# Kernel optimization log

Measured on AMD Instinct MI355X. Metric: run time of the kernel, lower is better.

The kernel has to match this reference:

```python
import jax, jax.numpy as jnp
import numpy as np

N, F_IN, HID, EMB, K = 4096, 1433, 256, 16, 10
ALPHA = 0.2   # LeakyReLU negative slope
V = 1.0       # Student-t degrees of freedom
NEG_INF = -9e15


def _xavier(key, shape):
    std = (2.0 / (shape[0] + shape[1])) ** 0.5
    return std * jax.random.normal(key, shape, dtype=jnp.float32)


def setup_inputs() -> dict:
    key = jax.random.key(0)
    ks = jax.random.split(key, 10)
    x = jax.random.normal(ks[0], (N, F_IN), dtype=jnp.float32)
    adj = (jax.random.uniform(ks[1], (N, N)) < 0.01).astype(jnp.float32)
    adj = jnp.maximum(adj, jnp.eye(N, dtype=jnp.float32))
    M = jax.random.uniform(ks[2], (N, N), dtype=jnp.float32)  # proximity matrix
    return {
        "x": x,
        "adj": adj,
        "M": M,
        "W1": _xavier(ks[3], (F_IN, HID)),
        "a_self1": _xavier(ks[4], (HID, 1)),
        "a_neigh1": _xavier(ks[5], (HID, 1)),
        "W2": _xavier(ks[6], (HID, EMB)),
        "a_self2": _xavier(ks[7], (EMB, 1)),
        "a_neigh2": _xavier(ks[8], (EMB, 1)),
        "cluster_layer": _xavier(ks[9], (K, EMB)),
    }


def _gat_layer(h_in, adj, M, W, a_self, a_neigh):
    h = h_in @ W                                   # [N, D]
    # dense attention logits: self score broadcast over rows + neighbor score over cols
    logits = (h @ a_self) + (h @ a_neigh).T        # [N, N]
    logits = jax.nn.leaky_relu(logits * M, negative_slope=ALPHA)
    logits = jnp.where(adj > 0, logits, NEG_INF)
    attention = jax.nn.softmax(logits, axis=1)     # row-stochastic
    return jax.nn.elu(attention @ h)               # concat=True -> ELU


def reference(x, adj, M, W1, a_self1, a_neigh1, W2, a_self2, a_neigh2, cluster_layer):
    h = _gat_layer(x, adj, M, W1, a_self1, a_neigh1)
    h = _gat_layer(h, adj, M, W2, a_self2, a_neigh2)
    # F.normalize(h, p=2, dim=1) with eps clamp
    z = h / jnp.maximum(jnp.linalg.norm(h, axis=1, keepdims=True), 1e-12)
    A_pred = jax.nn.sigmoid(z @ z.T)               # [N, N] dot-product decoder
    # Student-t soft assignment (get_Q)
    dist2 = jnp.sum((z[:, None, :] - cluster_layer[None, :, :]) ** 2, axis=2)  # [N, K]
    q = 1.0 / (1.0 + dist2 / V)
    q = q ** ((V + 1.0) / 2.0)
    q = q / jnp.sum(q, axis=1, keepdims=True)
    return A_pred, z, q
```

## Files before the change

### kernel.cpp

```cpp
#include <hip/hip_runtime.h>
#include <hip/hip_bf16.h>

#define NN 4096
#define FIN 1433
#define HID 256
#define EMB 16
#define KCL 10
#define CAP 256
#define ALPHA_LR 0.2f
#define KP 1472
#define NT (KP / 64)

typedef __attribute__((ext_vector_type(8))) short bf16x8;
typedef __attribute__((ext_vector_type(8))) short s16x8;
typedef __attribute__((ext_vector_type(4))) float f32x4;

__device__ __align__(16) short g_xb[(size_t)NN * KP];
__device__ __align__(16) short g_w1t[(size_t)HID * KP];
__device__ __align__(16) float g_h1[(size_t)NN * HID];
__device__ __align__(16) float g_s1[NN];
__device__ __align__(16) float g_n1[NN];
__device__ __align__(16) int   g_cnt[NN];
__device__ __align__(16) int   g_cols[(size_t)NN * CAP];
__device__ __align__(16) float g_mv[(size_t)NN * CAP];
__device__ __align__(16) float g_h2[(size_t)NN * EMB];
__device__ __align__(16) float g_s2[NN];
__device__ __align__(16) float g_n2[NN];
__device__ __align__(16) float g_z[(size_t)NN * EMB];

__device__ __forceinline__ short f2bf(float f) {
    union { float f; unsigned u; } v; v.f = f;
    unsigned r = v.u + 0x7fffu + ((v.u >> 16) & 1u);
    return (short)(r >> 16);
}
__device__ __forceinline__ float eluf(float v) { return v > 0.f ? v : __expf(v) - 1.f; }

__launch_bounds__(256)
__global__ void k_cast(const float* __restrict__ x, const float* __restrict__ W1) {
    int b = blockIdx.x, tid = threadIdx.x;
    if (b < NN) {
        const float* src = x + (size_t)b * FIN;
        short* dst = g_xb + (size_t)b * KP;
        for (int j = tid; j < KP; j += 256)
            dst[j] = (j < FIN) ? f2bf(src[j]) : (short)0;
    } else {
        int n = b - NN;
        short* dst = g_w1t + (size_t)n * KP;
        for (int k = tid; k < KP; k += 256)
            dst[k] = (k < FIN) ? f2bf(W1[(size_t)k * HID + n]) : (short)0;
    }
}

__launch_bounds__(256)
__global__ void k_gemm1b() {
    __shared__ short As[2][32][72];
    __shared__ short Bs[2][64][72];
    int bid = blockIdx.x;
    int rt = bid >> 2, nt = bid & 3;
    int row0 = rt * 32, n0 = nt * 64;
    int tid = threadIdx.x, lane = tid & 63, w = tid >> 6;
    int wm = w >> 1, wn = w & 1;
    int arow = tid >> 3, acol = (tid & 7) * 8;
    int brow = tid >> 2, bcol = (tid & 3) * 16;
    const short* xptr = g_xb  + (size_t)(row0 + arow) * KP + acol;
    const short* wptr = g_w1t + (size_t)(n0 + brow) * KP + bcol;
    f32x4 acc0 = {0.f,0.f,0.f,0.f}, acc1 = {0.f,0.f,0.f,0.f};

    s16x8 a_r  = *(const s16x8*)xptr;
    s16x8 b_r0 = *(const s16x8*)wptr;
    s16x8 b_r1 = *(const s16x8*)(wptr + 8);
    *(s16x8*)&As[0][arow][acol]     = a_r;
    *(s16x8*)&Bs[0][brow][bcol]     = b_r0;
    *(s16x8*)&Bs[0][brow][bcol + 8] = b_r1;
    __syncthreads();

    int fr = lane & 15, fk = (lane >> 4) * 8;
    for (int t = 0; t < NT; ++t) {
        int cur = t & 1;
        if (t + 1 < NT) {
            a_r  = *(const s16x8*)(xptr + (t + 1) * 64);
            b_r0 = *(const s16x8*)(wptr + (t + 1) * 64);
            b_r1 = *(const s16x8*)(wptr + (t + 1) * 64 + 8);
        }
        #pragma unroll
        for (int kk = 0; kk < 2; ++kk) {
            bf16x8 af  = *(const bf16x8*)&As[cur][wm * 16 + fr][fk + kk * 32];
            bf16x8 bf0 = *(const bf16x8*)&Bs[cur][wn * 32 + fr][fk + kk * 32];
            bf16x8 bf1 = *(const bf16x8*)&Bs[cur][wn * 32 + 16 + fr][fk + kk * 32];
            acc0 = __builtin_amdgcn_mfma_f32_16x16x32_bf16(af, bf0, acc0, 0, 0, 0);
            acc1 = __builtin_amdgcn_mfma_f32_16x16x32_bf16(af, bf1, acc1, 0, 0, 0);
        }
        if (t + 1 < NT) {
            *(s16x8*)&As[cur ^ 1][arow][acol]     = a_r;
            *(s16x8*)&Bs[cur ^ 1][brow][bcol]     = b_r0;
            *(s16x8*)&Bs[cur ^ 1][brow][bcol + 8] = b_r1;
            __syncthreads();
        }
    }
    int rowb = (lane >> 4) * 4;
    #pragma unroll
    for (int t = 0; t < 4; ++t) {
        int grow = row0 + wm * 16 + rowb + t;
        g_h1[(size_t)grow * HID + n0 + wn * 32 + fr]      = acc0[t];
        g_h1[(size_t)grow * HID + n0 + wn * 32 + 16 + fr] = acc1[t];
    }
}

__launch_bounds__(256)
__global__ void k_sn1(const float* __restrict__ a_s, const float* __restrict__ a_n) {
    int row = blockIdx.x * 4 + (threadIdx.x >> 6);
    int lane = threadIdx.x & 63;
    const float* r = g_h1 + (size_t)row * HID;
    float ss = 0.f, sn = 0.f;
    #pragma unroll
    for (int q = 0; q < 4; ++q) {
        float hv = r[lane + 64 * q];
        ss += hv * a_s[lane + 64 * q];
        sn += hv * a_n[lane + 64 * q];
    }
    #pragma unroll
    for (int o = 32; o; o >>= 1) { ss += __shfl_xor(ss, o); sn += __shfl_xor(sn, o); }
    if (lane == 0) { g_s1[row] = ss; g_n1[row] = sn; }
}

__launch_bounds__(256)
__global__ void k_csr(const float* __restrict__ adj, const float* __restrict__ M) {
    __shared__ int lc[4][CAP];
    int w = threadIdx.x >> 6;
    int row = blockIdx.x * 4 + w;
    int lane = threadIdx.x & 63;
    const float* Arow = adj + (size_t)row * NN;
    unsigned long long lmask = (1ull << lane) - 1ull;
    int base = 0;
    #pragma unroll
    for (int it = 0; it < 16; it += 4) {
        int j0 = it * 256 + lane * 4;
        f32x4 A0 = *(const f32x4*)&Arow[j0];
        f32x4 A1 = *(const f32x4*)&Arow[j0 + 256];
        f32x4 A2 = *(const f32x4*)&Arow[j0 + 512];
        f32x4 A3 = *(const f32x4*)&Arow[j0 + 768];
        f32x4 blk[4] = {A0, A1, A2, A3};
        #pragma unroll
        for (int b = 0; b < 4; ++b) {
            #pragma unroll
            for (int q = 0; q < 4; ++q) {
                bool nz = blk[b][q] > 0.f;
                unsigned long long bal = __ballot(nz);
                if (nz) {
                    int pos = base + __popcll(bal & lmask);
                    if (pos < CAP) lc[w][pos] = j0 + b * 256 + q;
                }
                base += __popcll(bal);
            }
        }
    }
    int nnz = base < CAP ? base : CAP;
    if (lane == 0) g_cnt[row] = nnz;
    __syncthreads();
    const float* Mrow = M + (size_t)row * NN;
    for (int k = lane; k < nnz; k += 64) {
        int col = lc[w][k];
        g_cols[(size_t)row * CAP + k] = col;
        g_mv[(size_t)row * CAP + k]   = Mrow[col];
    }
}

__launch_bounds__(256)
__global__ void k_attn1s(const float* __restrict__ W2,
                         const float* __restrict__ as2, const float* __restrict__ an2) {
    int w = threadIdx.x >> 6, lane = threadIdx.x & 63;
    int row = blockIdx.x * 4 + w;
    int nnz = g_cnt[row];
    if (nnz > 128) nnz = 128;
    float s_i = g_s1[row];
    const int* cp = g_cols + (size_t)row * CAP;
    const float* mp = g_mv + (size_t)row * CAP;
    int c0 = 0, c1 = 0;
    float lg0 = -INFINITY, lg1 = -INFINITY;
    if (lane < nnz) {
        c0 = cp[lane];
        float t = (s_i + g_n1[c0]) * mp[lane];
        lg0 = t > 0.f ? t : ALPHA_LR * t;
    }
    if (lane + 64 < nnz) {
        c1 = cp[lane + 64];
        float t = (s_i + g_n1[c1]) * mp[lane + 64];
        lg1 = t > 0.f ? t : ALPHA_LR * t;
    }
    float mx = fmaxf(lg0, lg1);
    #pragma unroll
    for (int o = 32; o; o >>= 1) mx = fmaxf(mx, __shfl_xor(mx, o));
    float p0 = (lane < nnz)      ? __expf(lg0 - mx) : 0.f;
    float p1 = (lane + 64 < nnz) ? __expf(lg1 - mx) : 0.f;
    float sm = p0 + p1;
    #pragma unroll
    for (int o = 32; o; o >>= 1) sm += __shfl_xor(sm, o);
    float inv = 1.f / sm;

    f32x4 acc = {0.f, 0.f, 0.f, 0.f};
    int kmax = nnz < 64 ? nnz : 64;
    #pragma unroll 4
    for (int k = 0; k < kmax; ++k) {
        float p = __shfl(p0, k);
        int   c = __shfl(c0, k);
        acc += p * *(const f32x4*)&g_h1[(size_t)c * HID + lane * 4];
    }
    if (nnz > 64) {
        int k2 = nnz - 64;
        #pragma unroll 4
        for (int k = 0; k < k2; ++k) {
            float p = __shfl(p1, k);
            int   c = __shfl(c1, k);
            acc += p * *(const f32x4*)&g_h1[(size_t)c * HID + lane * 4];
        }
    }
    f32x4 o1;
    #pragma unroll
    for (int j = 0; j < 4; ++j) o1[j] = eluf(acc[j] * inv);

    float part[16];
    #pragma unroll
    for (int e = 0; e < 16; ++e) part[e] = 0.f;
    #pragma unroll
    for (int j = 0; j < 4; ++j) {
        const f32x4* wr = (const f32x4*)&W2[(size_t)(lane * 4 + j) * EMB];
        f32x4 w0 = wr[0], w1 = wr[1], w2 = wr[2], w3 = wr[3];
        float ov = o1[j];
        #pragma unroll
        for (int e = 0; e < 4; ++e) {
            part[e]      += ov * w0[e];
            part[4 + e]  += ov * w1[e];
            part[8 + e]  += ov * w2[e];
            part[12 + e] += ov * w3[e];
        }
    }
    #pragma unroll
    for (int o = 32; o; o >>= 1)
        #pragma unroll
        for (int e = 0; e < 16; ++e) part[e] += __shfl_xor(part[e], o);
    if (lane == 0) {
        float ps = 0.f, pn = 0.f;
        float* h2p = g_h2 + (size_t)row * EMB;
        #pragma unroll
        for (int e = 0; e < 16; ++e) {
            h2p[e] = part[e];
            ps += part[e] * as2[e];
            pn += part[e] * an2[e];
        }
        g_s2[row] = ps; g_n2[row] = pn;
    }
}

__launch_bounds__(256)
__global__ void k_attn2s(const float* __restrict__ cl,
                         float* __restrict__ zo, float* __restrict__ qo) {
    int row = blockIdx.x * 4 + (threadIdx.x >> 6);
    int lane = threadIdx.x & 63;
    int kq = lane >> 4, c = lane & 15;
    int nnz = g_cnt[row];
    float s_i = g_s2[row];
    const int* cp = g_cols + (size_t)row * CAP;
    const float* mp = g_mv + (size_t)row * CAP;
    float mx = -INFINITY;
    for (int k = kq; k < nnz; k += 4) {
        float t = (s_i + g_n2[cp[k]]) * mp[k];
        mx = fmaxf(mx, t > 0.f ? t : ALPHA_LR * t);
    }
    mx = fmaxf(mx, __shfl_xor(mx, 16));
    mx = fmaxf(mx, __shfl_xor(mx, 32));
    float l = 0.f, acc = 0.f;
    for (int k = kq; k < nnz; k += 4) {
        int colk = cp[k];
        float t = (s_i + g_n2[colk]) * mp[k];
        float p = __expf((t > 0.f ? t : ALPHA_LR * t) - mx);
        l += p;
        acc += p * g_h2[(size_t)colk * EMB + c];
    }
    l += __shfl_xor(l, 16);  l += __shfl_xor(l, 32);
    acc += __shfl_xor(acc, 16); acc += __shfl_xor(acc, 32);
    float h = eluf(acc / l);
    float ss = h * h;
    ss += __shfl_xor(ss, 1); ss += __shfl_xor(ss, 2);
    ss += __shfl_xor(ss, 4); ss += __shfl_xor(ss, 8);
    float z = h * (1.f / fmaxf(sqrtf(ss), 1e-12f));
    if (kq == 0) { g_z[(size_t)row * EMB + c] = z; zo[(size_t)row * EMB + c] = z; }
    float qv[KCL]; float qs = 0.f;
    #pragma unroll
    for (int k2 = 0; k2 < KCL; ++k2) {
        float d = z - cl[k2 * EMB + c];
        float d2 = d * d;
        d2 += __shfl_xor(d2, 1); d2 += __shfl_xor(d2, 2);
        d2 += __shfl_xor(d2, 4); d2 += __shfl_xor(d2, 8);
        float t = 1.f / (1.f + d2);
        qv[k2] = t; qs += t;
    }
    if (kq == 0 && c < KCL) {
        float myq = 0.f;
        #pragma unroll
        for (int k2 = 0; k2 < KCL; ++k2) if (c == k2) myq = qv[k2];
        qo[(size_t)row * KCL + c] = myq / qs;
    }
}

__launch_bounds__(256)
__global__ void k_apred(float* __restrict__ out) {
    __shared__ float za[128][17];
    __shared__ float zb[128][17];
    int bx = blockIdx.x & 31, by = blockIdx.x >> 5;
    int tid = threadIdx.x;
    {
        int idx = tid * 8;
        int row = idx >> 4;
        int e = idx & 15;
        const f32x4* sa = (const f32x4*)(g_z + (size_t)(by * 128 + row) * EMB + e);
        const f32x4* sb = (const f32x4*)(g_z + (size_t)(bx * 128 + row) * EMB + e);
        f32x4 a0 = sa[0], a1 = sa[1], b0 = sb[0], b1 = sb[1];
        #pragma unroll
        for (int t = 0; t < 4; ++t) {
            za[row][e + t] = a0[t]; za[row][e + 4 + t] = a1[t];
            zb[row][e + t] = b0[t]; zb[row][e + 4 + t] = b1[t];
        }
    }
    __syncthreads();
    int tr = tid >> 4, tc = tid & 15;
    float acc[8][8];
    #pragma unroll
    for (int r = 0; r < 8; ++r)
        #pragma unroll
        for (int c = 0; c < 8; ++c) acc[r][c] = 0.f;
    for (int e = 0; e < 16; ++e) {
        float ra[8], rb[8];
        #pragma unroll
        for (int r = 0; r < 8; ++r) ra[r] = za[tr * 8 + r][e];
        #pragma unroll
        for (int c = 0; c < 8; ++c) rb[c] = zb[tc * 8 + c][e];
        #pragma unroll
        for (int r = 0; r < 8; ++r)
            #pragma unroll
            for (int c = 0; c < 8; ++c) acc[r][c] += ra[r] * rb[c];
    }
    #pragma unroll
    for (int r = 0; r < 8; ++r) {
        f32x4 lo, hi;
        #pragma unroll
        for (int c = 0; c < 4; ++c) {
            lo[c] = 1.f / (1.f + __expf(-acc[r][c]));
            hi[c] = 1.f / (1.f + __expf(-acc[r][c + 4]));
        }
        float* dst = &out[(size_t)(by * 128 + tr * 8 + r) * NN + bx * 128 + tc * 8];
        *(f32x4*)dst = lo;
        *(f32x4*)(dst + 4) = hi;
    }
}

extern "C" void kernel_launch(void* const* d_in, const int* in_sizes, int n_in,
                              void* d_out, int out_size, void* d_ws, size_t ws_size,
                              hipStream_t stream) {
    (void)in_sizes; (void)n_in; (void)d_ws; (void)ws_size; (void)out_size;
    const float* x   = (const float*)d_in[0];
    const float* adj = (const float*)d_in[1];
    const float* M   = (const float*)d_in[2];
    const float* W1  = (const float*)d_in[3];
    const float* as1 = (const float*)d_in[4];
    const float* an1 = (const float*)d_in[5];
    const float* W2  = (const float*)d_in[6];
    const float* as2 = (const float*)d_in[7];
    const float* an2 = (const float*)d_in[8];
    const float* cl  = (const float*)d_in[9];

    float* outA = (float*)d_out;
    float* outZ = outA + (size_t)NN * NN;
    float* outQ = outZ + (size_t)NN * EMB;

    hipLaunchKernelGGL(k_cast,   dim3(NN + HID), dim3(256), 0, stream, x, W1);
    hipLaunchKernelGGL(k_gemm1b, dim3(512),      dim3(256), 0, stream);
    hipLaunchKernelGGL(k_sn1,    dim3(1024),     dim3(256), 0, stream, as1, an1);
    hipLaunchKernelGGL(k_csr,    dim3(1024),     dim3(256), 0, stream, adj, M);
    hipLaunchKernelGGL(k_attn1s, dim3(1024),     dim3(256), 0, stream, W2, as2, an2);
    hipLaunchKernelGGL(k_attn2s, dim3(1024),     dim3(256), 0, stream, cl, outZ, outQ);
    hipLaunchKernelGGL(k_apred,  dim3(1024),     dim3(256), 0, stream, outA);
}
```

Measured before the change: 266.7 us.

## Fuse CSR construction into first attention kernel using LDS atomic compaction

Merges the adjacency-to-CSR kernel into the layer-1 attention kernel so the column list and M values are built and consumed in the same block, removing a launch and the reread of the compacted arrays. Compaction switches from wave ballot/popcount to shared-memory atomic counters, and adjacency loads are batched eight vectors at a time. Column order within a row becomes nondeterministic, which changes floating-point summation order, and atomics may serialize on dense rows.

```diff
diff --git a/kernel.cpp b/kernel.cpp
--- a/kernel.cpp
+++ b/kernel.cpp
@@ -124,69 +124,60 @@
 }
 
 __launch_bounds__(256)
-__global__ void k_csr(const float* __restrict__ adj, const float* __restrict__ M) {
+__global__ void k_attn1s(const float* __restrict__ adj, const float* __restrict__ M,
+                         const float* __restrict__ W2,
+                         const float* __restrict__ as2, const float* __restrict__ an2) {
     __shared__ int lc[4][CAP];
-    int w = threadIdx.x >> 6;
+    __shared__ int cnts[4];
+    int w = threadIdx.x >> 6, lane = threadIdx.x & 63;
     int row = blockIdx.x * 4 + w;
-    int lane = threadIdx.x & 63;
+    if (lane == 0) cnts[w] = 0;
+    __syncthreads();
+
     const float* Arow = adj + (size_t)row * NN;
-    unsigned long long lmask = (1ull << lane) - 1ull;
-    int base = 0;
-    #pragma unroll
-    for (int it = 0; it < 16; it += 4) {
-        int j0 = it * 256 + lane * 4;
-        f32x4 A0 = *(const f32x4*)&Arow[j0];
-        f32x4 A1 = *(const f32x4*)&Arow[j0 + 256];
-        f32x4 A2 = *(const f32x4*)&Arow[j0 + 512];
-        f32x4 A3 = *(const f32x4*)&Arow[j0 + 768];
-        f32x4 blk[4] = {A0, A1, A2, A3};
-        #pragma unroll
-        for (int b = 0; b < 4; ++b) {
+    #pragma unroll
+    for (int it = 0; it < 16; it += 8) {
+        f32x4 A[8];
+        #pragma unroll
+        for (int u = 0; u < 8; ++u)
+            A[u] = *(const f32x4*)&Arow[(it + u) * 256 + lane * 4];
+        #pragma unroll
+        for (int u = 0; u < 8; ++u) {
+            int j0 = (it + u) * 256 + lane * 4;
             #pragma unroll
             for (int q = 0; q < 4; ++q) {
-                bool nz = blk[b][q] > 0.f;
-                unsigned long long bal = __ballot(nz);
-                if (nz) {
-                    int pos = base + __popcll(bal & lmask);
-                    if (pos < CAP) lc[w][pos] = j0 + b * 256 + q;
+                if (A[u][q] > 0.f) {
+                    int pos = atomicAdd(&cnts[w], 1);
+                    if (pos < CAP) lc[w][pos] = j0 + q;
                 }
-                base += __popcll(bal);
             }
         }
     }
-    int nnz = base < CAP ? base : CAP;
-    if (lane == 0) g_cnt[row] = nnz;
     __syncthreads();
+    int nnzC = cnts[w]; if (nnzC > CAP) nnzC = CAP;
+    if (lane == 0) g_cnt[row] = nnzC;
+
     const float* Mrow = M + (size_t)row * NN;
-    for (int k = lane; k < nnz; k += 64) {
-        int col = lc[w][k];
-        g_cols[(size_t)row * CAP + k] = col;
-        g_mv[(size_t)row * CAP + k]   = Mrow[col];
-    }
-}
-
-__launch_bounds__(256)
-__global__ void k_attn1s(const float* __restrict__ W2,
-                         const float* __restrict__ as2, const float* __restrict__ an2) {
-    int w = threadIdx.x >> 6, lane = threadIdx.x & 63;
-    int row = blockIdx.x * 4 + w;
-    int nnz = g_cnt[row];
-    if (nnz > 128) nnz = 128;
     float s_i = g_s1[row];
-    const int* cp = g_cols + (size_t)row * CAP;
-    const float* mp = g_mv + (size_t)row * CAP;
     int c0 = 0, c1 = 0;
     float lg0 = -INFINITY, lg1 = -INFINITY;
-    if (lane < nnz) {
-        c0 = cp[lane];
-        float t = (s_i + g_n1[c0]) * mp[lane];
-        lg0 = t > 0.f ? t : ALPHA_LR * t;
-    }
-    if (lane + 64 < nnz) {
-        c1 = cp[lane + 64];
-        float t = (s_i + g_n1[c1]) * mp[lane + 64];
-        lg1 = t > 0.f ? t : ALPHA_LR * t;
-    }
+    #pragma unroll
+    for (int t = 0; t < 4; ++t) {
+        int k = lane + 64 * t;
+        if (k < nnzC) {
+            int c = lc[w][k];
+            float mv = Mrow[c];
+            g_cols[(size_t)row * CAP + k] = c;
+            g_mv[(size_t)row * CAP + k]   = mv;
+            if (t < 2) {
+                float tt = (s_i + g_n1[c]) * mv;
+                float lg = tt > 0.f ? tt : ALPHA_LR * tt;
+                if (t == 0) { c0 = c; lg0 = lg; } else { c1 = c; lg1 = lg; }
+            }
+        }
+    }
+    int nnz = nnzC > 128 ? 128 : nnzC;
+
     float mx = fmaxf(lg0, lg1);
     #pragma unroll
     for (int o = 32; o; o >>= 1) mx = fmaxf(mx, __shfl_xor(mx, o));
@@ -375,8 +366,7 @@
     hipLaunchKernelGGL(k_cast,   dim3(NN + HID), dim3(256), 0, stream, x, W1);
     hipLaunchKernelGGL(k_gemm1b, dim3(512),      dim3(256), 0, stream);
     hipLaunchKernelGGL(k_sn1,    dim3(1024),     dim3(256), 0, stream, as1, an1);
-    hipLaunchKernelGGL(k_csr,    dim3(1024),     dim3(256), 0, stream, adj, M);
-    hipLaunchKernelGGL(k_attn1s, dim3(1024),     dim3(256), 0, stream, W2, as2, an2);
+    hipLaunchKernelGGL(k_attn1s, dim3(1024),     dim3(256), 0, stream, adj, M, W2, as2, an2);
     hipLaunchKernelGGL(k_attn2s, dim3(1024),     dim3(256), 0, stream, cl, outZ, outQ);
     hipLaunchKernelGGL(k_apred,  dim3(1024),     dim3(256), 0, stream, outA);
 }
```

New measurement: 261.7 us. About the same (-1.9%).
